# Kernel optimization log

Hardware: AMD Instinct MI355X
Metric: run time of the kernel (lower is better)

The kernel has to match this reference:

```python
import jax, jax.numpy as jnp
import numpy as np


def setup_inputs() -> dict:
    key = jax.random.key(0)
    ks = jax.random.split(key, 5)
    B, N, Fin, Fout = 8, 2048, 512, 512
    stdv = 1.0 / np.sqrt(Fout)
    w_stdv = 1.0 / np.sqrt(Fin)
    x = jax.random.normal(ks[0], (B, N, Fin), dtype=jnp.float32)
    weight = jax.random.uniform(ks[1], (Fin, Fout), dtype=jnp.float32, minval=-stdv, maxval=stdv)
    bias = jax.random.uniform(ks[2], (Fout,), dtype=jnp.float32, minval=-stdv, maxval=stdv)
    w_one = jax.random.uniform(ks[3], (Fin, Fin), dtype=jnp.float32, minval=-w_stdv, maxval=w_stdv)
    w_two = jax.random.uniform(ks[4], (Fin, Fin), dtype=jnp.float32, minval=-w_stdv, maxval=w_stdv)
    return {"x": x, "weight": weight, "bias": bias, "w_one": w_one, "w_two": w_two}


def reference(x, weight, bias, w_one, w_two):
    # x: [B, N, Fin]
    support = jnp.einsum('bnf,fo->bno', x, weight)          # [B, N, Fout]
    phi_one = jnp.einsum('ef,bnf->ben', w_one, x)           # [B, Fin, N]
    phi_two = jnp.einsum('ef,bnf->ben', w_two, x)           # [B, Fin, N]
    adj = jnp.einsum('ben,bem->bnm', phi_one, phi_two)      # [B, N, N]
    adj = jax.nn.softmax(adj, axis=1)                        # softmax over dim=1 (columns)
    out = jnp.einsum('bnm,bmo->bno', adj, support)           # [B, N, Fout]
    return out + bias
```

## Files before the change

### kernel.cpp

```cpp
#include <hip/hip_runtime.h>
#include <math.h>

#define BB 8
#define NN 2048
#define FF 512

typedef __attribute__((ext_vector_type(8))) short short8;
typedef __attribute__((ext_vector_type(4))) float floatx4;

__device__ __forceinline__ unsigned short f2bf(float f) {
    union { float f; unsigned u; } v; v.f = f;
    unsigned r = v.u + 0x7FFFu + ((v.u >> 16) & 1u);
    return (unsigned short)(r >> 16);
}

__global__ __launch_bounds__(256) void gemm_mfma_bt(
    const unsigned short* __restrict__ A, const unsigned short* __restrict__ B,
    void* __restrict__ Cv, const float* __restrict__ bias, float* __restrict__ Dsum,
    int M, int Nc, int K, int a_ld, int b_ld, int ldc,
    long a_batch, long b_batch, long c_batch, int mode)
{
    __shared__ __align__(16) unsigned short Alds[128 * 32];
    __shared__ __align__(16) unsigned short Blds[128 * 32];

    const int tid  = threadIdx.x;
    const int wave = tid >> 6;
    const int lane = tid & 63;
    const int bz   = blockIdx.z;

    const unsigned short* Ab = A + (long)bz * a_batch;
    const unsigned short* Bb = B + (long)bz * b_batch;

    const int m0 = blockIdx.y * 128;
    const int n0 = blockIdx.x * 128;

    const int wm   = (wave >> 1) * 64;
    const int wn   = (wave & 1) * 64;
    const int fl   = lane & 15;
    const int quad = lane >> 4;

    floatx4 acc[4][4] = {};

    for (int k0 = 0; k0 < K; k0 += 32) {
        #pragma unroll
        for (int issue = 0; issue < 2; ++issue) {
            const int cbase = issue * 256 + wave * 64;
            const int c = cbase + lane;
            const int row = c >> 2, kq = (c & 3) * 8;
            const unsigned short* gA = Ab + (long)(m0 + row) * a_ld + k0 + kq;
            __builtin_amdgcn_global_load_lds(
                (const __attribute__((address_space(1))) void*)gA,
                (__attribute__((address_space(3))) void*)&Alds[cbase * 8], 16, 0, 0);
            const unsigned short* gB = Bb + (long)(n0 + row) * b_ld + k0 + kq;
            __builtin_amdgcn_global_load_lds(
                (const __attribute__((address_space(1))) void*)gB,
                (__attribute__((address_space(3))) void*)&Blds[cbase * 8], 16, 0, 0);
        }
        __syncthreads();

        short8 af[4], bf[4];
        #pragma unroll
        for (int i = 0; i < 4; ++i)
            af[i] = *(const short8*)&Alds[(wm + i * 16 + fl) * 32 + quad * 8];
        #pragma unroll
        for (int j = 0; j < 4; ++j)
            bf[j] = *(const short8*)&Blds[(wn + j * 16 + fl) * 32 + quad * 8];

        #pragma unroll
        for (int i = 0; i < 4; ++i)
            #pragma unroll
            for (int j = 0; j < 4; ++j)
                acc[i][j] = __builtin_amdgcn_mfma_f32_16x16x32_bf16(af[i], bf[j], acc[i][j], 0, 0, 0);
        __syncthreads();
    }

    if (mode == 0) {
        float* Cb = (float*)Cv + (long)bz * c_batch;
        #pragma unroll
        for (int j = 0; j < 4; ++j) {
            const int ng = n0 + wn + j * 16 + fl;
            const float badd = bias ? bias[ng] : 0.0f;
            #pragma unroll
            for (int i = 0; i < 4; ++i) {
                const int mg = m0 + wm + i * 16 + quad * 4;
                #pragma unroll
                for (int r = 0; r < 4; ++r)
                    Cb[(long)(mg + r) * ldc + ng] = acc[i][j][r] + badd;
            }
        }
    } else if (mode == 1) {
        unsigned short* Cb = (unsigned short*)Cv + (long)bz * c_batch;
        #pragma unroll
        for (int j = 0; j < 4; ++j) {
            const int ng = n0 + wn + j * 16 + fl;
            #pragma unroll
            for (int i = 0; i < 4; ++i) {
                const int mg = m0 + wm + i * 16 + quad * 4;
                #pragma unroll
                for (int r = 0; r < 4; ++r)
                    Cb[(long)(mg + r) * ldc + ng] = f2bf(acc[i][j][r]);
            }
        }
    } else {
        unsigned short* Cb = (unsigned short*)Cv + (long)bz * c_batch;
        float* Db = Dsum + (long)bz * NN;
        #pragma unroll
        for (int j = 0; j < 4; ++j) {
            const int ng = n0 + wn + j * 16 + fl;
            float csum = 0.f;
            #pragma unroll
            for (int i = 0; i < 4; ++i) {
                const int mg = m0 + wm + i * 16 + quad * 4;
                #pragma unroll
                for (int r = 0; r < 4; ++r) {
                    const float e = __expf(acc[i][j][r]);
                    csum += e;
                    Cb[(long)(mg + r) * ldc + ng] = f2bf(e);
                }
            }
            csum += __shfl_xor(csum, 16);
            csum += __shfl_xor(csum, 32);
            if (quad == 0) atomicAdd(&Db[ng], csum);
        }
    }
}

__global__ __launch_bounds__(256) void convert_all(
    const float* __restrict__ x, const float* __restrict__ w1, const float* __restrict__ w2,
    unsigned short* __restrict__ xb, unsigned short* __restrict__ w1b, unsigned short* __restrict__ w2b)
{
    const long NX = (long)BB * NN * FF / 8;
    const long NW = (long)FF * FF / 8;
    long t = (long)blockIdx.x * 256 + threadIdx.x;
    const float* in; unsigned short* out;
    if (t < NX) { in = x; out = xb; }
    else if (t < NX + NW) { in = w1; out = w1b; t -= NX; }
    else if (t < NX + 2 * NW) { in = w2; out = w2b; t -= NX + NW; }
    else return;
    const long i = t * 8;
    float4 a = *(const float4*)(in + i);
    float4 b = *(const float4*)(in + i + 4);
    short8 o;
    o[0] = (short)f2bf(a.x); o[1] = (short)f2bf(a.y);
    o[2] = (short)f2bf(a.z); o[3] = (short)f2bf(a.w);
    o[4] = (short)f2bf(b.x); o[5] = (short)f2bf(b.y);
    o[6] = (short)f2bf(b.z); o[7] = (short)f2bf(b.w);
    *(short8*)(out + i) = o;
}

__global__ __launch_bounds__(256) void transpose_convert(
    const float* __restrict__ in, unsigned short* __restrict__ out, int dim)
{
    __shared__ float t[32][33];
    const int tx = threadIdx.x & 31, ty = threadIdx.x >> 5;
    const int x0 = blockIdx.x * 32, y0 = blockIdx.y * 32;
    #pragma unroll
    for (int k = 0; k < 32; k += 8)
        t[ty + k][tx] = in[(long)(y0 + ty + k) * dim + x0 + tx];
    __syncthreads();
    #pragma unroll
    for (int k = 0; k < 32; k += 8)
        out[(long)(x0 + ty + k) * dim + y0 + tx] = f2bf(t[tx][ty + k]);
}

__global__ __launch_bounds__(256) void zero_f32(float* __restrict__ p, long n)
{
    long i = (long)blockIdx.x * 256 + threadIdx.x;
    if (i < n) p[i] = 0.0f;
}

__global__ __launch_bounds__(256) void scale_transpose(
    const unsigned short* __restrict__ Call, const float* __restrict__ D,
    unsigned short* __restrict__ supT, int batch0)
{
    __shared__ float t[32][33];
    __shared__ float rD[32];
    const int tx = threadIdx.x & 31, ty = threadIdx.x >> 5;
    const int mt = blockIdx.x * 32, ot = blockIdx.y * 32;
    const int b = batch0 + blockIdx.z;
    const unsigned short* Cb = Call + (long)b * NN * 1536;
    unsigned short* Tb = supT + (long)b * NN * FF;
    if (threadIdx.x < 32) rD[threadIdx.x] = 1.0f / D[(long)b * NN + mt + threadIdx.x];
    #pragma unroll
    for (int k = 0; k < 32; k += 8) {
        unsigned short u = Cb[(long)(mt + ty + k) * 1536 + 1024 + ot + tx];
        union { unsigned u; float f; } cv; cv.u = ((unsigned)u) << 16;
        t[ty + k][tx] = cv.f;
    }
    __syncthreads();
    #pragma unroll
    for (int k = 0; k < 32; k += 8)
        Tb[(long)(ot + ty + k) * NN + mt + tx] = f2bf(t[tx][ty + k] * rD[tx]);
}

extern "C" void kernel_launch(void* const* d_in, const int* in_sizes, int n_in,
                              void* d_out, int out_size, void* d_ws, size_t ws_size,
                              hipStream_t stream)
{
    const float* x      = (const float*)d_in[0];
    const float* weight = (const float*)d_in[1];
    const float* bias   = (const float*)d_in[2];
    const float* w_one  = (const float*)d_in[3];
    const float* w_two  = (const float*)d_in[4];
    float* out = (float*)d_out;

    const long NF  = (long)NN * FF;
    const long NN2 = (long)NN * NN;
    const long CROW = 1536;

    char* p = (char*)d_ws;
    unsigned short* xb    = (unsigned short*)p; p += (size_t)BB * NF * 2;
    unsigned short* Wall  = (unsigned short*)p; p += (size_t)CROW * FF * 2;
    unsigned short* Call  = (unsigned short*)p; p += (size_t)BB * NN * CROW * 2;
    unsigned short* supT  = (unsigned short*)p; p += (size_t)BB * NF * 2;
    float*          Dsum  = (float*)p;          p += (size_t)BB * NN * 4;
    unsigned short* E     = (unsigned short*)p;
    unsigned short* w1b = Wall;
    unsigned short* w2b = Wall + (size_t)FF * FF;
    unsigned short* wTb = Wall + (size_t)2 * FF * FF;

    const size_t fixed = (size_t)(p - (char*)d_ws);
    const bool full = ws_size >= fixed + (size_t)BB * NN2 * 2;

    dim3 blk(256);

    convert_all<<<dim3(4352), blk, 0, stream>>>(x, w_one, w_two, xb, w1b, w2b);
    transpose_convert<<<dim3(FF / 32, FF / 32), blk, 0, stream>>>(weight, wTb, FF);
    zero_f32<<<dim3((BB * NN) / 256), blk, 0, stream>>>(Dsum, BB * NN);

    gemm_mfma_bt<<<dim3(CROW / 128, NN / 128, BB), blk, 0, stream>>>(
        xb, Wall, Call, nullptr, nullptr, NN, CROW, FF,
        FF, FF, CROW, NF, 0, NN * CROW, 1);

    if (full) {
        gemm_mfma_bt<<<dim3(NN / 128, NN / 128, BB), blk, 0, stream>>>(
            Call, Call + FF, E, nullptr, Dsum, NN, NN, FF,
            CROW, CROW, NN, NN * CROW, NN * CROW, NN2, 2);
        scale_transpose<<<dim3(NN / 32, FF / 32, BB), blk, 0, stream>>>(Call, Dsum, supT, 0);
        gemm_mfma_bt<<<dim3(FF / 128, NN / 128, BB), blk, 0, stream>>>(
            E, supT, out, bias, nullptr, NN, FF, NN,
            NN, NN, FF, NN2, NF, NF, 0);
    } else {
        for (int b = 0; b < BB; ++b) {
            const unsigned short* Cb = Call + (size_t)b * NN * CROW;
            gemm_mfma_bt<<<dim3(NN / 128, NN / 128, 1), blk, 0, stream>>>(
                Cb, Cb + FF, E, nullptr, Dsum + (size_t)b * NN, NN, NN, FF,
                CROW, CROW, NN, 0, 0, 0, 2);
            scale_transpose<<<dim3(NN / 32, FF / 32, 1), blk, 0, stream>>>(Call, Dsum, supT, b);
            gemm_mfma_bt<<<dim3(FF / 128, NN / 128, 1), blk, 0, stream>>>(
                E, supT + (size_t)b * NF, out + (size_t)b * NF, bias, nullptr, NN, FF, NN,
                NN, NN, FF, 0, 0, 0, 0);
        }
    }
}
```

Baseline: 264.7 us.

## Swizzle LDS tiles and swap GEMM operands for vectorized transposed epilogue stores

```diff
diff --git a/kernel.cpp b/kernel.cpp
--- a/kernel.cpp
+++ b/kernel.cpp
@@ -7,6 +7,7 @@
 
 typedef __attribute__((ext_vector_type(8))) short short8;
 typedef __attribute__((ext_vector_type(4))) float floatx4;
+typedef __attribute__((ext_vector_type(4))) unsigned short ushort4v;
 
 __device__ __forceinline__ unsigned short f2bf(float f) {
     union { float f; unsigned u; } v; v.f = f;
@@ -16,7 +17,7 @@
 
 __global__ __launch_bounds__(256) void gemm_mfma_bt(
     const unsigned short* __restrict__ A, const unsigned short* __restrict__ B,
-    void* __restrict__ Cv, const float* __restrict__ bias, float* __restrict__ Dsum,
+    void* __restrict__ Ov, const float* __restrict__ bias, float* __restrict__ Dsum,
     int M, int Nc, int K, int a_ld, int b_ld, int ldc,
     long a_batch, long b_batch, long c_batch, int mode)
 {
@@ -39,6 +40,9 @@
     const int fl   = lane & 15;
     const int quad = lane >> 4;
 
+    const int src_kq0 = ((lane & 3) ^ ((lane >> 3) & 3)) * 8;
+    const int jsw = (quad ^ ((fl >> 1) & 3)) * 8;
+
     floatx4 acc[4][4] = {};
 
     for (int k0 = 0; k0 < K; k0 += 32) {
@@ -46,7 +50,9 @@
         for (int issue = 0; issue < 2; ++issue) {
             const int cbase = issue * 256 + wave * 64;
             const int c = cbase + lane;
-            const int row = c >> 2, kq = (c & 3) * 8;
+            const int row = c >> 2;
+            const int kq = ((c & 3) ^ ((c >> 3) & 3)) * 8;
+            (void)src_kq0;
             const unsigned short* gA = Ab + (long)(m0 + row) * a_ld + k0 + kq;
             __builtin_amdgcn_global_load_lds(
                 (const __attribute__((address_space(1))) void*)gA,
@@ -61,10 +67,10 @@
         short8 af[4], bf[4];
         #pragma unroll
         for (int i = 0; i < 4; ++i)
-            af[i] = *(const short8*)&Alds[(wm + i * 16 + fl) * 32 + quad * 8];
+            af[i] = *(const short8*)&Alds[(wm + i * 16 + fl) * 32 + jsw];
         #pragma unroll
         for (int j = 0; j < 4; ++j)
-            bf[j] = *(const short8*)&Blds[(wn + j * 16 + fl) * 32 + quad * 8];
+            bf[j] = *(const short8*)&Blds[(wn + j * 16 + fl) * 32 + jsw];
 
         #pragma unroll
         for (int i = 0; i < 4; ++i)
@@ -75,52 +81,68 @@
     }
 
     if (mode == 0) {
-        float* Cb = (float*)Cv + (long)bz * c_batch;
+        float* Ob = (float*)Ov + (long)bz * c_batch;
         #pragma unroll
         for (int j = 0; j < 4; ++j) {
             const int ng = n0 + wn + j * 16 + fl;
-            const float badd = bias ? bias[ng] : 0.0f;
             #pragma unroll
             for (int i = 0; i < 4; ++i) {
                 const int mg = m0 + wm + i * 16 + quad * 4;
+                float4 b4 = *(const float4*)&bias[mg];
+                float4 v;
+                v.x = acc[i][j][0] + b4.x; v.y = acc[i][j][1] + b4.y;
+                v.z = acc[i][j][2] + b4.z; v.w = acc[i][j][3] + b4.w;
+                *(float4*)&Ob[(long)ng * ldc + mg] = v;
+            }
+        }
+    } else if (mode == 1) {
+        unsigned short* Ob = (unsigned short*)Ov + (long)bz * c_batch;
+        #pragma unroll
+        for (int j = 0; j < 4; ++j) {
+            const int ng = n0 + wn + j * 16 + fl;
+            #pragma unroll
+            for (int i = 0; i < 4; ++i) {
+                const int mg = m0 + wm + i * 16 + quad * 4;
+                ushort4v o;
+                o[0] = f2bf(acc[i][j][0]); o[1] = f2bf(acc[i][j][1]);
+                o[2] = f2bf(acc[i][j][2]); o[3] = f2bf(acc[i][j][3]);
+                *(ushort4v*)&Ob[(long)ng * ldc + mg] = o;
+            }
+        }
+    } else {
+        unsigned short* Ob = (unsigned short*)Ov + (long)bz * c_batch;
+        float* Db = Dsum + (long)bz * NN;
+        #pragma unroll
+        for (int i = 0; i < 4; ++i)
+            #pragma unroll
+            for (int j = 0; j < 4; ++j)
                 #pragma unroll
                 for (int r = 0; r < 4; ++r)
-                    Cb[(long)(mg + r) * ldc + ng] = acc[i][j][r] + badd;
-            }
-        }
-    } else if (mode == 1) {
-        unsigned short* Cb = (unsigned short*)Cv + (long)bz * c_batch;
+                    acc[i][j][r] = __expf(acc[i][j][r]);
         #pragma unroll
         for (int j = 0; j < 4; ++j) {
             const int ng = n0 + wn + j * 16 + fl;
             #pragma unroll
             for (int i = 0; i < 4; ++i) {
                 const int mg = m0 + wm + i * 16 + quad * 4;
-                #pragma unroll
-                for (int r = 0; r < 4; ++r)
-                    Cb[(long)(mg + r) * ldc + ng] = f2bf(acc[i][j][r]);
-            }
-        }
-    } else {
-        unsigned short* Cb = (unsigned short*)Cv + (long)bz * c_batch;
-        float* Db = Dsum + (long)bz * NN;
-        #pragma unroll
-        for (int j = 0; j < 4; ++j) {
-            const int ng = n0 + wn + j * 16 + fl;
-            float csum = 0.f;
-            #pragma unroll
-            for (int i = 0; i < 4; ++i) {
-                const int mg = m0 + wm + i * 16 + quad * 4;
-                #pragma unroll
-                for (int r = 0; r < 4; ++r) {
-                    const float e = __expf(acc[i][j][r]);
-                    csum += e;
-                    Cb[(long)(mg + r) * ldc + ng] = f2bf(e);
-                }
-            }
-            csum += __shfl_xor(csum, 16);
-            csum += __shfl_xor(csum, 32);
-            if (quad == 0) atomicAdd(&Db[ng], csum);
+                ushort4v o;
+                o[0] = f2bf(acc[i][j][0]); o[1] = f2bf(acc[i][j][1]);
+                o[2] = f2bf(acc[i][j][2]); o[3] = f2bf(acc[i][j][3]);
+                *(ushort4v*)&Ob[(long)ng * ldc + mg] = o;
+            }
+        }
+        #pragma unroll
+        for (int i = 0; i < 4; ++i) {
+            #pragma unroll
+            for (int r = 0; r < 4; ++r) {
+                float rs = acc[i][0][r] + acc[i][1][r] + acc[i][2][r] + acc[i][3][r];
+                rs += __shfl_xor(rs, 1);
+                rs += __shfl_xor(rs, 2);
+                rs += __shfl_xor(rs, 4);
+                rs += __shfl_xor(rs, 8);
+                if (fl == 0)
+                    atomicAdd(&Db[m0 + wm + i * 16 + quad * 4 + r], rs);
+            }
         }
     }
 }
@@ -181,10 +203,11 @@
     const unsigned short* Cb = Call + (long)b * NN * 1536;
     unsigned short* Tb = supT + (long)b * NN * FF;
     if (threadIdx.x < 32) rD[threadIdx.x] = 1.0f / D[(long)b * NN + mt + threadIdx.x];
+    __syncthreads();
     #pragma unroll
     for (int k = 0; k < 32; k += 8) {
         unsigned short u = Cb[(long)(mt + ty + k) * 1536 + 1024 + ot + tx];
-        union { unsigned u; float f; } cv; cv.u = ((unsigned)u) << 16;
+        union { unsigned uu; float f; } cv; cv.uu = ((unsigned)u) << 16;
         t[ty + k][tx] = cv.f;
     }
     __syncthreads();
@@ -228,27 +251,27 @@
     transpose_convert<<<dim3(FF / 32, FF / 32), blk, 0, stream>>>(weight, wTb, FF);
     zero_f32<<<dim3((BB * NN) / 256), blk, 0, stream>>>(Dsum, BB * NN);
 
-    gemm_mfma_bt<<<dim3(CROW / 128, NN / 128, BB), blk, 0, stream>>>(
-        xb, Wall, Call, nullptr, nullptr, NN, CROW, FF,
-        FF, FF, CROW, NF, 0, NN * CROW, 1);
+    gemm_mfma_bt<<<dim3(NN / 128, CROW / 128, BB), blk, 0, stream>>>(
+        Wall, xb, Call, nullptr, nullptr, (int)CROW, NN, FF,
+        FF, FF, (int)CROW, 0, NF, NN * CROW, 1);
 
     if (full) {
         gemm_mfma_bt<<<dim3(NN / 128, NN / 128, BB), blk, 0, stream>>>(
-            Call, Call + FF, E, nullptr, Dsum, NN, NN, FF,
-            CROW, CROW, NN, NN * CROW, NN * CROW, NN2, 2);
+            Call + FF, Call, E, nullptr, Dsum, NN, NN, FF,
+            (int)CROW, (int)CROW, NN, NN * CROW, NN * CROW, NN2, 2);
         scale_transpose<<<dim3(NN / 32, FF / 32, BB), blk, 0, stream>>>(Call, Dsum, supT, 0);
-        gemm_mfma_bt<<<dim3(FF / 128, NN / 128, BB), blk, 0, stream>>>(
-            E, supT, out, bias, nullptr, NN, FF, NN,
-            NN, NN, FF, NN2, NF, NF, 0);
+        gemm_mfma_bt<<<dim3(NN / 128, FF / 128, BB), blk, 0, stream>>>(
+            supT, E, out, bias, nullptr, FF, NN, NN,
+            NN, NN, FF, NF, NN2, NF, 0);
     } else {
         for (int b = 0; b < BB; ++b) {
             const unsigned short* Cb = Call + (size_t)b * NN * CROW;
             gemm_mfma_bt<<<dim3(NN / 128, NN / 128, 1), blk, 0, stream>>>(
-                Cb, Cb + FF, E, nullptr, Dsum + (size_t)b * NN, NN, NN, FF,
-                CROW, CROW, NN, 0, 0, 0, 2);
+                Cb + FF, Cb, E, nullptr, Dsum + (size_t)b * NN, NN, NN, FF,
+                (int)CROW, (int)CROW, NN, 0, 0, 0, 2);
             scale_transpose<<<dim3(NN / 32, FF / 32, 1), blk, 0, stream>>>(Call, Dsum, supT, b);
-            gemm_mfma_bt<<<dim3(FF / 128, NN / 128, 1), blk, 0, stream>>>(
-                E, supT + (size_t)b * NF, out + (size_t)b * NF, bias, nullptr, NN, FF, NN,
+            gemm_mfma_bt<<<dim3(NN / 128, FF / 128, 1), blk, 0, stream>>>(
+                supT + (size_t)b * NF, E, out + (size_t)b * NF, bias, nullptr, FF, NN, NN,
                 NN, NN, FF, 0, 0, 0, 0);
         }
     }
```

After: 302.2 us. 1.14x slower.
